# Kernel optimization log

Hardware: AMD Instinct MI355X
Metric: run time of the kernel (lower is better)

## Reference

```python
import jax, jax.numpy as jnp
import numpy as np

K_TOTAL = 48
NUM_RINGS = 3
RING_K = K_TOTAL // NUM_RINGS
RADIUS = 50.0
NUM_HEADS = 4


def setup_inputs() -> dict:
    key = jax.random.key(0)
    ks = jax.random.split(key, 12)
    B, N, Fin, D = 2, 4096, 256, 256
    H = D // 2
    features = jax.random.normal(ks[0], (B, N, Fin), jnp.float32)
    xy = jax.random.uniform(ks[1], (B, N, 2), jnp.float32) * 200.0
    t = jax.random.uniform(ks[2], (B, N, 1), jnp.float32) * 100.0
    coords = jnp.concatenate([xy, t], -1)

    def lin(k, fan_out, fan_in):
        bound = 1.0 / np.sqrt(fan_in)
        kw, kb = jax.random.split(k)
        W = jax.random.uniform(kw, (fan_out, fan_in), jnp.float32, -bound, bound)
        b = jax.random.uniform(kb, (fan_out,), jnp.float32, -bound, bound)
        return W, b

    Wfeat, bfeat = lin(ks[3], D, Fin)
    Wpe1, bpe1 = lin(ks[4], H, 4)
    Wpe2, bpe2 = lin(ks[5], D, H)
    Win, bin_ = lin(ks[6], 3 * D, D)
    Wout, bout = lin(ks[7], D, D)
    Wg1, bg1 = lin(ks[8], 32, 4)
    Wg2, bg2 = lin(ks[9], NUM_RINGS, 32)
    gamma = jnp.ones((D,), jnp.float32)
    beta = jnp.zeros((D,), jnp.float32)
    return dict(features=features, coords=coords, Wfeat=Wfeat, bfeat=bfeat,
                Wpe1=Wpe1, bpe1=bpe1, Wpe2=Wpe2, bpe2=bpe2,
                Win=Win, bin_=bin_, Wout=Wout, bout=bout,
                Wg1=Wg1, bg1=bg1, Wg2=Wg2, bg2=bg2, gamma=gamma, beta=beta)


def _safe_norm(x):
    # median over a size-1 last dim equals x itself (matches torch path)
    denom = jnp.median(x, axis=-1, keepdims=True) + 1e-6
    return jnp.clip(x / denom, 0.0, 10.0)


def _encode_one(bf, bc, p):
    N, D = bf.shape
    inf = jnp.float32(jnp.inf)
    # --- pairwise KNN: spatial + 0.3*|dt|, causal + radius + no-self ---
    diff = bc[:, None, :] - bc[None, :, :]                  # (N,N,3)
    sd = jnp.sqrt(jnp.sum(diff[..., :2] ** 2, -1))          # (N,N)
    dist = sd + 0.3 * jnp.abs(diff[..., 2])
    t = bc[:, 2]
    bad = jnp.eye(N, dtype=bool) | (t[None, :] > t[:, None]) | (sd > RADIUS)
    dist = jnp.where(bad, inf, dist)
    neg_top, idx = jax.lax.top_k(-dist, K_TOTAL)            # K smallest
    kdist_raw = -neg_top                                    # (N,K) ascending
    valid = jnp.isfinite(kdist_raw)
    kdist = jnp.where(valid, kdist_raw, 0.0)
    # --- neighbor gather + relative positional encoding ---
    neigh = bf[idx]                                         # (N,K,D)
    ncoord = bc[idx]                                        # (N,K,3)
    rel = jnp.concatenate([ncoord - bc[:, None, :], kdist[..., None]], -1)
    pe = jax.nn.relu(rel @ p['Wpe1'].T + p['bpe1']) @ p['Wpe2'].T + p['bpe2']
    neigh = neigh + pe
    # --- per-ring masked MHA (shared weights across rings) ---
    R, Kr, Hh = NUM_RINGS, RING_K, NUM_HEADS
    hd = D // Hh
    kr = neigh.reshape(N, R, Kr, D)
    vr = valid.reshape(N, R, Kr)
    Wq, Wk, Wv = p['Win'][:D], p['Win'][D:2 * D], p['Win'][2 * D:]
    bq, bk, bv = p['bin_'][:D], p['bin_'][D:2 * D], p['bin_'][2 * D:]
    q = (bf @ Wq.T + bq).reshape(N, Hh, hd) / jnp.sqrt(jnp.float32(hd))
    k = (kr @ Wk.T + bk).reshape(N, R, Kr, Hh, hd)
    v = (kr @ Wv.T + bv).reshape(N, R, Kr, Hh, hd)
    logits = jnp.einsum('nhd,nrkhd->nrhk', q, k)
    logits = jnp.where(vr[:, :, None, :], logits, -1e9)
    attn = jax.nn.softmax(logits, axis=-1)
    out = jnp.einsum('nrhk,nrkhd->nrhd', attn, v).reshape(N, R, D)
    out = out @ p['Wout'].T + p['bout']
    ring_any = vr.any(-1)                                   # (N,R)
    aggs = jnp.where(ring_any[..., None], out, 0.0)
    # --- ring gate from local density / time structure ---
    vc = jnp.maximum(valid.sum(-1), 1)                      # (N,)
    dens = jnp.take_along_axis(kdist, (vc - 1)[:, None], axis=1)
    dens_n = _safe_norm(dens)[:, 0]
    ratio = jnp.clip(vc.astype(jnp.float32) / K_TOTAL, 0.0, 1.0)
    dt = jnp.abs(ncoord[..., 2] - t[:, None])
    dtm = jnp.where(valid, dt, 0.0)
    denom = vc.astype(jnp.float32)
    dt_mean = dtm.sum(-1) / denom
    dt_sq = jnp.where(valid, (dt - dt_mean[:, None]) ** 2, 0.0)
    dt_std = jnp.sqrt(dt_sq.sum(-1) / denom + 1e-8)
    gate_in = jnp.stack([dens_n, ratio,
                         _safe_norm(dt_mean[:, None])[:, 0],
                         _safe_norm(dt_std[:, None])[:, 0]], -1)
    glog = jax.nn.relu(gate_in @ p['Wg1'].T + p['bg1']) @ p['Wg2'].T + p['bg2']
    glog = jnp.where(ring_any, glog, -inf)
    no_nb = ~ring_any.any(-1)
    special = jnp.where(jnp.arange(R) == 0, 10.0, 0.0).astype(jnp.float32)
    glog = jnp.where(no_nb[:, None], special[None, :], glog)
    w = jax.nn.softmax(glog, axis=-1)
    fused = jnp.einsum('nr,nrd->nd', w, aggs)
    # --- residual + layernorm (dropout is identity in eval) ---
    x = bf + fused
    mu = x.mean(-1, keepdims=True)
    var = x.var(-1, keepdims=True)
    return (x - mu) / jnp.sqrt(var + 1e-5) * p['gamma'] + p['beta']


def reference(features, coords, Wfeat, bfeat, Wpe1, bpe1, Wpe2, bpe2,
              Win, bin_, Wout, bout, Wg1, bg1, Wg2, bg2, gamma, beta):
    p = dict(Wpe1=Wpe1, bpe1=bpe1, Wpe2=Wpe2, bpe2=bpe2, Win=Win, bin_=bin_,
             Wout=Wout, bout=bout, Wg1=Wg1, bg1=bg1, Wg2=Wg2, bg2=bg2,
             gamma=gamma, beta=beta)
    feat_proj = features @ Wfeat.T + bfeat                  # (B,N,D)
    return jax.vmap(lambda f, c: _encode_one(f, c, p))(feat_proj, coords)
```

## Files before the change

### kernel.cpp

```cpp
#include <hip/hip_runtime.h>
#include <cmath>

#define NPTS 4096
#define NB   8192
#define DM   256
#define KK   48

__global__ __launch_bounds__(128) void prep_wkv2(
    const float* __restrict__ Win, const float* __restrict__ Wpe2,
    const float* __restrict__ bpe2, const float* __restrict__ bin_,
    float* __restrict__ Wk2, float* __restrict__ Wv2,
    float* __restrict__ bkf, float* __restrict__ bvf)
{
    const int o = blockIdx.x;
    const int j = threadIdx.x;
    const float* wk = Win + (size_t)(256 + o) * 256;
    const float* wv = Win + (size_t)(512 + o) * 256;
    float ak = 0.f, av = 0.f;
    for (int d = 0; d < 256; ++d) {
        float pw = Wpe2[(size_t)d * 128 + j];
        ak = fmaf(wk[d], pw, ak);
        av = fmaf(wv[d], pw, av);
    }
    Wk2[(size_t)o * 128 + j] = ak;
    Wv2[(size_t)o * 128 + j] = av;

    __shared__ float pk[128], pv[128];
    pk[j] = wk[j] * bpe2[j] + wk[j + 128] * bpe2[j + 128];
    pv[j] = wv[j] * bpe2[j] + wv[j + 128] * bpe2[j + 128];
    __syncthreads();
    for (int off = 64; off >= 1; off >>= 1) {
        if (j < off) { pk[j] += pk[j + off]; pv[j] += pv[j + off]; }
        __syncthreads();
    }
    if (j == 0) {
        bkf[o] = bin_[256 + o] + pk[0];
        bvf[o] = bin_[512 + o] + pv[0];
    }
}

__global__ __launch_bounds__(256) void prep_wqw2(
    const float* __restrict__ Win, const float* __restrict__ Wk2,
    const float* __restrict__ bin_,
    float* __restrict__ WqW2, float* __restrict__ bqW2)
{
    const int o = blockIdx.x;
    const int h = o >> 7, j = o & 127;
    const int d = threadIdx.x;
    float acc = 0.f;
    for (int dp = 0; dp < 64; ++dp) {
        const float w2 = Wk2[(size_t)(64 * h + dp) * 128 + j];
        acc = fmaf(Win[(size_t)(64 * h + dp) * 256 + d], w2, acc);
    }
    WqW2[(size_t)o * 256 + d] = acc * 0.125f;
    if (d < 64) {
        float pb = bin_[64 * h + d] * Wk2[(size_t)(64 * h + d) * 128 + j];
        #pragma unroll
        for (int off = 1; off < 64; off <<= 1) pb += __shfl_xor(pb, off);
        if (d == 0) bqW2[o] = pb * 0.125f;
    }
}

__global__ __launch_bounds__(256) void prep_wcat(
    const float* __restrict__ Wout, const float* __restrict__ Wv2,
    float* __restrict__ Wcat)
{
    const int o = blockIdx.x;
    const int t = threadIdx.x;
    Wcat[(size_t)o * 768 + t] = Wout[(size_t)o * 256 + t];
    for (int v = t; v < 512; v += 256) {
        const int h = v >> 7, jj = v & 127;
        const float* wo  = Wout + (size_t)o * 256 + h * 64;
        const float* wv2 = Wv2 + (size_t)(h * 64) * 128 + jj;
        float a = 0.f;
        for (int dp = 0; dp < 64; ++dp) a = fmaf(wo[dp], wv2[(size_t)dp * 128], a);
        Wcat[(size_t)o * 768 + 256 + v] = a;
    }
}

#define GEMM_BODY(XPTR, XSTRIDE, WPTR, KDIM, R0, C0)                          \
    __shared__ float xs[32][65];                                              \
    __shared__ float wsd[32][65];                                             \
    const int tid = threadIdx.x;                                              \
    const int lm = tid >> 5, lk = tid & 31;                                   \
    const int rr = 4 * (tid & 15), cc = 4 * (tid >> 4);                       \
    float acc[4][4] = {{0.f,0.f,0.f,0.f},{0.f,0.f,0.f,0.f},                   \
                       {0.f,0.f,0.f,0.f},{0.f,0.f,0.f,0.f}};                  \
    for (int k0 = 0; k0 < (KDIM); k0 += 32) {                                 \
        __syncthreads();                                                      \
        _Pragma("unroll")                                                     \
        for (int it = 0; it < 8; ++it) {                                      \
            const int m = lm + it * 8;                                        \
            xs[lk][m]  = (XPTR)[(size_t)((R0) + m) * (XSTRIDE) + k0 + lk];    \
            wsd[lk][m] = (WPTR)[(size_t)((C0) + m) * (KDIM) + k0 + lk];       \
        }                                                                     \
        __syncthreads();                                                      \
        _Pragma("unroll")                                                     \
        for (int k = 0; k < 32; ++k) {                                        \
            const float4 xv = *(const float4*)&xs[k][rr];                     \
            const float4 wv = *(const float4*)&wsd[k][cc];                    \
            acc[0][0] = fmaf(xv.x, wv.x, acc[0][0]);                          \
            acc[0][1] = fmaf(xv.x, wv.y, acc[0][1]);                          \
            acc[0][2] = fmaf(xv.x, wv.z, acc[0][2]);                          \
            acc[0][3] = fmaf(xv.x, wv.w, acc[0][3]);                          \
            acc[1][0] = fmaf(xv.y, wv.x, acc[1][0]);                          \
            acc[1][1] = fmaf(xv.y, wv.y, acc[1][1]);                          \
            acc[1][2] = fmaf(xv.y, wv.z, acc[1][2]);                          \
            acc[1][3] = fmaf(xv.y, wv.w, acc[1][3]);                          \
            acc[2][0] = fmaf(xv.z, wv.x, acc[2][0]);                          \
            acc[2][1] = fmaf(xv.z, wv.y, acc[2][1]);                          \
            acc[2][2] = fmaf(xv.z, wv.z, acc[2][2]);                          \
            acc[2][3] = fmaf(xv.z, wv.w, acc[2][3]);                          \
            acc[3][0] = fmaf(xv.w, wv.x, acc[3][0]);                          \
            acc[3][1] = fmaf(xv.w, wv.y, acc[3][1]);                          \
            acc[3][2] = fmaf(xv.w, wv.z, acc[3][2]);                          \
            acc[3][3] = fmaf(xv.w, wv.w, acc[3][3]);                          \
        }                                                                     \
    }

__global__ __launch_bounds__(256) void gemm_plain(
    const float* __restrict__ X, int xstride,
    const float* __restrict__ W, const float* __restrict__ bias,
    float scale, float* __restrict__ Y, int ystride, int K, int ntiles)
{
    const int bid = blockIdx.x;
    const int r0 = (bid / ntiles) * 64;
    const int c0 = (bid % ntiles) * 64;
    GEMM_BODY(X, xstride, W, K, r0, c0)
    float b0 = 0.f, b1 = 0.f, b2 = 0.f, b3 = 0.f;
    if (bias) { b0 = bias[c0+cc+0]; b1 = bias[c0+cc+1]; b2 = bias[c0+cc+2]; b3 = bias[c0+cc+3]; }
    #pragma unroll
    for (int i = 0; i < 4; ++i) {
        float4 o;
        o.x = (acc[i][0] + b0) * scale;
        o.y = (acc[i][1] + b1) * scale;
        o.z = (acc[i][2] + b2) * scale;
        o.w = (acc[i][3] + b3) * scale;
        *(float4*)&Y[(size_t)(r0 + rr + i) * ystride + c0 + cc] = o;
    }
}

__global__ __launch_bounds__(256) void gemm_qkvw(
    const float* __restrict__ feat, const float* __restrict__ Win,
    const float* __restrict__ WqW2,
    const float* __restrict__ bin_, const float* __restrict__ bkf,
    const float* __restrict__ bvf, const float* __restrict__ bqW2,
    float* __restrict__ Qm, float* __restrict__ Kp,
    float* __restrict__ Vp, float* __restrict__ qWa)
{
    const int bid = blockIdx.x;
    const int r0 = (bid / 20) * 64;
    const int cg = (bid % 20) * 64;
    const float* Wb; const float* bb; float scale; float* Yb; int ys; int c0;
    if (cg < 256)      { Wb = Win;             bb = bin_; scale = 0.125f; Yb = Qm;  ys = 256; c0 = cg; }
    else if (cg < 512) { Wb = Win + 256 * 256; bb = bkf;  scale = 1.f;    Yb = Kp;  ys = 256; c0 = cg - 256; }
    else if (cg < 768) { Wb = Win + 512 * 256; bb = bvf;  scale = 1.f;    Yb = Vp;  ys = 256; c0 = cg - 512; }
    else               { Wb = WqW2;            bb = bqW2; scale = 1.f;    Yb = qWa; ys = 512; c0 = cg - 768; }
    GEMM_BODY(feat, 256, Wb, 256, r0, c0)
    const float b0 = bb[c0+cc+0], b1 = bb[c0+cc+1], b2 = bb[c0+cc+2], b3 = bb[c0+cc+3];
    #pragma unroll
    for (int i = 0; i < 4; ++i) {
        float4 o;
        o.x = (acc[i][0] + b0) * scale;
        o.y = (acc[i][1] + b1) * scale;
        o.z = (acc[i][2] + b2) * scale;
        o.w = (acc[i][3] + b3) * scale;
        *(float4*)&Yb[(size_t)(r0 + rr + i) * ys + c0 + cc] = o;
    }
}

#define GRPMIN(BASE, OUTKEY) do {                                            \
    unsigned m_ = 0xFFFFFFFFu; int ms_ = (BASE);                             \
    _Pragma("unroll")                                                        \
    for (int s_ = 0; s_ < 16; ++s_) {                                        \
        unsigned v_ = ((dead >> ((BASE) + s_)) & 1ull) ? 0xFFFFFFFFu         \
                                                       : db[(BASE) + s_];    \
        if (v_ < m_) { m_ = v_; ms_ = (BASE) + s_; }                         \
    }                                                                        \
    OUTKEY = ((unsigned long long)m_ << 32) | (unsigned)(ms_ * 64 + lane);   \
} while (0)

static __device__ __forceinline__ unsigned long long umin64(
    unsigned long long a, unsigned long long b) { return a < b ? a : b; }

static __device__ __forceinline__ unsigned long long shfl_xor_u64(
    unsigned long long v, int mask)
{
    unsigned lo = (unsigned)(v & 0xFFFFFFFFull);
    unsigned hi = (unsigned)(v >> 32);
    lo = (unsigned)__shfl_xor((int)lo, mask);
    hi = (unsigned)__shfl_xor((int)hi, mask);
    return ((unsigned long long)hi << 32) | lo;
}

__global__ __launch_bounds__(256) void knn_kernel(
    const float* __restrict__ coords, int* __restrict__ nidx, float* __restrict__ ndist)
{
    #pragma clang fp contract(off)
    const int lane = threadIdx.x & 63;
    const int p = blockIdx.x * 4 + (threadIdx.x >> 6);
    const int b = p >> 12;
    const int i = p & 4095;
    const float* cb = coords + (size_t)b * NPTS * 3;
    const float xi = cb[i * 3 + 0], yi = cb[i * 3 + 1], ti = cb[i * 3 + 2];

    unsigned db[64];
    #pragma unroll
    for (int s = 0; s < 64; ++s) {
        const int j = s * 64 + lane;
        const float xj = cb[j * 3 + 0], yj = cb[j * 3 + 1], tj = cb[j * 3 + 2];
        const float dx = xi - xj, dy = yi - yj;
        const float sd = sqrtf(dx * dx + dy * dy);
        const float dd = sd + 0.3f * fabsf(tj - ti);
        const bool bad = (j == i) || (tj > ti) || (sd > 50.0f);
        db[s] = bad ? 0x7F800000u : __float_as_uint(dd);
    }

    unsigned long long dead = 0ull;
    unsigned long long k0, k1, k2, k3;
    GRPMIN(0,  k0); GRPMIN(16, k1); GRPMIN(32, k2); GRPMIN(48, k3);
    unsigned long long lmin = umin64(umin64(k0, k1), umin64(k2, k3));

    unsigned long long reskey = 0ull;
    for (int k = 0; k < KK; ++k) {
        unsigned long long kb = lmin;
        #pragma unroll
        for (int off = 1; off < 64; off <<= 1) {
            unsigned long long o = shfl_xor_u64(kb, off);
            kb = o < kb ? o : kb;
        }
        if (lane == k) reskey = kb;
        const int wj = (int)(kb & 0xFFFFFFFFull);
        if ((wj & 63) == lane) {
            const int ws = wj >> 6;
            dead |= (1ull << ws);
            const int g = ws >> 4;
            if      (g == 0) GRPMIN(0,  k0);
            else if (g == 1) GRPMIN(16, k1);
            else if (g == 2) GRPMIN(32, k2);
            else             GRPMIN(48, k3);
            lmin = umin64(umin64(k0, k1), umin64(k2, k3));
        }
    }

    if (lane < KK) {
        ndist[(size_t)p * KK + lane] = __uint_as_float((unsigned)(reskey >> 32));
        nidx [(size_t)p * KK + lane] = (int)(reskey & 0xFFFFFFFFull);
    }
}

__global__ __launch_bounds__(256) void attn_kernel(
    const float* __restrict__ coords, const float* __restrict__ Q,
    const float* __restrict__ Kp, const float* __restrict__ Vp,
    const float* __restrict__ qWa,
    const int* __restrict__ nidx, const float* __restrict__ ndist,
    const float* __restrict__ Wpe1, const float* __restrict__ bpe1,
    const float* __restrict__ Wg1, const float* __restrict__ bg1,
    const float* __restrict__ Wg2, const float* __restrict__ bg2,
    float* __restrict__ vh, unsigned char* __restrict__ nonb)
{
    const int p = blockIdx.x;
    const int b = p >> 12;
    const int i = p & 4095;
    const int tid = threadIdx.x;

    __shared__ __align__(16) float qs[4][68];
    __shared__ __align__(16) float qw[4][132];
    __shared__ __align__(16) float rel[KK][4];
    __shared__ float kd[KK];
    __shared__ int   sidx[KK];
    __shared__ int   svalid[KK];
    __shared__ __align__(16) float hid[KK][132];
    __shared__ float wsh[KK][4];
    __shared__ float wring[4];

    for (int v = tid; v < 256; v += 256) qs[v >> 6][v & 63] = Q[(size_t)p * 256 + v];
    for (int v = tid; v < 512; v += 256) qw[v >> 7][v & 127] = qWa[(size_t)p * 512 + v];
    const float* cb = coords + (size_t)b * NPTS * 3;
    const float xi = cb[i * 3 + 0], yi = cb[i * 3 + 1], ti = cb[i * 3 + 2];
    if (tid < KK) {
        const float dd = ndist[(size_t)p * KK + tid];
        const int ix = nidx[(size_t)p * KK + tid];
        sidx[tid] = ix;
        const int val = (dd < 3.0e38f) ? 1 : 0;
        svalid[tid] = val;
        const float kdd = val ? dd : 0.f;
        kd[tid] = kdd;
        rel[tid][0] = cb[ix * 3 + 0] - xi;
        rel[tid][1] = cb[ix * 3 + 1] - yi;
        rel[tid][2] = cb[ix * 3 + 2] - ti;
        rel[tid][3] = kdd;
    }
    __syncthreads();

    if (tid < 64) {
        const int val = (tid < KK) ? svalid[tid] : 0;
        float dtv = 0.f;
        if (tid < KK && val) dtv = fabsf(rel[tid][2]);
        const unsigned long long m = __ballot(val != 0);
        const int count = __popcll(m);
        const int vc = count > 0 ? count : 1;
        float sdt = dtv;
        #pragma unroll
        for (int off = 1; off < 64; off <<= 1) sdt += __shfl_xor(sdt, off);
        const float vcf = (float)vc;
        const float dtmean = sdt / vcf;
        float dq = 0.f;
        if (tid < KK && val) { float tq = dtv - dtmean; dq = tq * tq; }
        float sdq = dq;
        #pragma unroll
        for (int off = 1; off < 64; off <<= 1) sdq += __shfl_xor(sdq, off);
        const float dtstd = sqrtf(sdq / vcf + 1e-8f);
        const float dens = kd[vc - 1];
        const float g0 = fminf(fmaxf(dens / (dens + 1e-6f), 0.f), 10.f);
        const float g1v = fminf(fmaxf(vcf / 48.f, 0.f), 1.f);
        const float g2 = fminf(fmaxf(dtmean / (dtmean + 1e-6f), 0.f), 10.f);
        const float g3 = fminf(fmaxf(dtstd / (dtstd + 1e-6f), 0.f), 10.f);
        float gh = 0.f;
        if (tid < 32) {
            gh = bg1[tid] + g0 * Wg1[tid * 4 + 0] + g1v * Wg1[tid * 4 + 1]
               + g2 * Wg1[tid * 4 + 2] + g3 * Wg1[tid * 4 + 3];
            gh = fmaxf(gh, 0.f);
        }
        float gl[3];
        #pragma unroll
        for (int r = 0; r < 3; ++r) {
            float part = (tid < 32) ? gh * Wg2[r * 32 + tid] : 0.f;
            #pragma unroll
            for (int off = 1; off < 64; off <<= 1) part += __shfl_xor(part, off);
            gl[r] = part + bg2[r];
        }
        if (count < 1)  gl[0] = -INFINITY;
        if (count < 17) gl[1] = -INFINITY;
        if (count < 33) gl[2] = -INFINITY;
        float w0 = 0.f, w1 = 0.f, w2 = 0.f;
        if (count > 0) {
            const float mx = fmaxf(gl[0], fmaxf(gl[1], gl[2]));
            const float e0 = expf(gl[0] - mx), e1 = expf(gl[1] - mx), e2 = expf(gl[2] - mx);
            const float es = e0 + e1 + e2;
            w0 = e0 / es; w1 = e1 / es; w2 = e2 / es;
        }
        if (tid == 0) {
            wring[0] = w0; wring[1] = w1; wring[2] = w2;
            nonb[p] = (count == 0) ? (unsigned char)1 : (unsigned char)0;
        }
    }
    for (int v = tid; v < KK * 128; v += 256) {
        const int s = v >> 7, jj = v & 127;
        const float4 r4 = *(const float4*)(&rel[s][0]);
        const float4 w4 = *(const float4*)(Wpe1 + (size_t)jj * 4);
        float hdd = bpe1[jj] + r4.x * w4.x + r4.y * w4.y + r4.z * w4.z + r4.w * w4.w;
        hid[s][jj] = fmaxf(hdd, 0.f);
    }
    __syncthreads();

    if (tid < 192) {
        const int s_ = tid >> 2, h_ = tid & 3;
        float acc = 0.f;
        const float4* hp = (const float4*)(&hid[s_][0]);
        const float4* qp = (const float4*)(&qw[h_][0]);
        #pragma unroll
        for (int j4 = 0; j4 < 32; ++j4) {
            float4 hv = hp[j4], qv = qp[j4];
            acc = fmaf(qv.x, hv.x, fmaf(qv.y, hv.y, fmaf(qv.z, hv.z, fmaf(qv.w, hv.w, acc))));
        }
        const float* kr = Kp + ((size_t)b * NPTS + sidx[s_]) * 256 + h_ * 64;
        const float4* qsp = (const float4*)(&qs[h_][0]);
        #pragma unroll
        for (int d4 = 0; d4 < 16; ++d4) {
            float4 kv = *(const float4*)(kr + d4 * 4);
            float4 qv = qsp[d4];
            acc = fmaf(qv.x, kv.x, fmaf(qv.y, kv.y, fmaf(qv.z, kv.z, fmaf(qv.w, kv.w, acc))));
        }
        float logit = svalid[s_] ? acc : -1e9f;
        float mx = logit;
        #pragma unroll
        for (int off = 4; off < 64; off <<= 1) mx = fmaxf(mx, __shfl_xor(mx, off));
        const float e = expf(logit - mx);
        float es = e;
        #pragma unroll
        for (int off = 4; off < 64; off <<= 1) es += __shfl_xor(es, off);
        wsh[s_][h_] = (e / es) * wring[tid >> 6];
    }
    __syncthreads();

    {
        const int h = tid >> 6, dp = tid & 63;
        const size_t bb = (size_t)b * NPTS;
        const float* vpb = Vp + h * 64 + dp;
        float a0 = 0.f, a1 = 0.f, a2 = 0.f, a3 = 0.f;
        #pragma unroll
        for (int s = 0; s < 12; ++s) {
            a0 = fmaf(wsh[s     ][h], vpb[(bb + sidx[s     ]) * 256], a0);
            a1 = fmaf(wsh[s + 12][h], vpb[(bb + sidx[s + 12]) * 256], a1);
            a2 = fmaf(wsh[s + 24][h], vpb[(bb + sidx[s + 24]) * 256], a2);
            a3 = fmaf(wsh[s + 36][h], vpb[(bb + sidx[s + 36]) * 256], a3);
        }
        vh[(size_t)p * 768 + tid] = (a0 + a1) + (a2 + a3);
    }
    for (int v = tid; v < 512; v += 256) {
        const int h = v >> 7, jj = v & 127;
        float a0 = 0.f, a1 = 0.f;
        #pragma unroll
        for (int s = 0; s < 24; ++s) {
            a0 = fmaf(wsh[s     ][h], hid[s     ][jj], a0);
            a1 = fmaf(wsh[s + 24][h], hid[s + 24][jj], a1);
        }
        vh[(size_t)p * 768 + 256 + v] = a0 + a1;
    }
}

__global__ __launch_bounds__(256) void ln_kernel(
    const float* __restrict__ xo, const float* __restrict__ feat,
    const float* __restrict__ bout, const unsigned char* __restrict__ nonb,
    const float* __restrict__ gamma, const float* __restrict__ beta,
    float* __restrict__ out)
{
    const int lane = threadIdx.x & 63;
    const int p = blockIdx.x * 4 + (threadIdx.x >> 6);
    const float4 xv = *(const float4*)&xo  [(size_t)p * 256 + lane * 4];
    const float4 fv = *(const float4*)&feat[(size_t)p * 256 + lane * 4];
    const float4 bv = *(const float4*)&bout[lane * 4];
    const float bm = nonb[p] ? 0.f : 1.f;
    float x0 = xv.x + fv.x + bm * bv.x;
    float x1 = xv.y + fv.y + bm * bv.y;
    float x2 = xv.z + fv.z + bm * bv.z;
    float x3 = xv.w + fv.w + bm * bv.w;
    float s1 = x0 + x1 + x2 + x3;
    float s2 = fmaf(x0, x0, fmaf(x1, x1, fmaf(x2, x2, x3 * x3)));
    #pragma unroll
    for (int off = 1; off < 64; off <<= 1) {
        s1 += __shfl_xor(s1, off);
        s2 += __shfl_xor(s2, off);
    }
    const float mu = s1 * (1.f / 256.f);
    const float var = s2 * (1.f / 256.f) - mu * mu;
    const float rs = 1.f / sqrtf(var + 1e-5f);
    const float4 gv = *(const float4*)&gamma[lane * 4];
    const float4 tv = *(const float4*)&beta [lane * 4];
    float4 o;
    o.x = (x0 - mu) * rs * gv.x + tv.x;
    o.y = (x1 - mu) * rs * gv.y + tv.y;
    o.z = (x2 - mu) * rs * gv.z + tv.z;
    o.w = (x3 - mu) * rs * gv.w + tv.w;
    *(float4*)&out[(size_t)p * 256 + lane * 4] = o;
}

extern "C" void kernel_launch(void* const* d_in, const int* in_sizes, int n_in,
                              void* d_out, int out_size, void* d_ws, size_t ws_size,
                              hipStream_t stream) {
    (void)in_sizes; (void)n_in; (void)out_size; (void)ws_size;
    const float* features = (const float*)d_in[0];
    const float* coords   = (const float*)d_in[1];
    const float* Wfeat    = (const float*)d_in[2];
    const float* bfeat    = (const float*)d_in[3];
    const float* Wpe1     = (const float*)d_in[4];
    const float* bpe1     = (const float*)d_in[5];
    const float* Wpe2     = (const float*)d_in[6];
    const float* bpe2     = (const float*)d_in[7];
    const float* Win      = (const float*)d_in[8];
    const float* bin_     = (const float*)d_in[9];
    const float* Wout     = (const float*)d_in[10];
    const float* bout     = (const float*)d_in[11];
    const float* Wg1      = (const float*)d_in[12];
    const float* bg1      = (const float*)d_in[13];
    const float* Wg2      = (const float*)d_in[14];
    const float* bg2      = (const float*)d_in[15];
    const float* gamma    = (const float*)d_in[16];
    const float* beta     = (const float*)d_in[17];
    float* out = (float*)d_out;

    float* ws   = (float*)d_ws;
    float* feat = ws;
    float* Qm   = feat + (size_t)NB * DM;
    float* Kp   = Qm   + (size_t)NB * DM;
    float* Vp   = Kp   + (size_t)NB * DM;
    float* qWa  = Vp   + (size_t)NB * DM;
    float* vh   = qWa  + (size_t)NB * 512;
    float* Wk2  = vh   + (size_t)NB * 768;
    float* Wv2  = Wk2  + 256 * 128;
    float* Wcat = Wv2  + 256 * 128;
    float* WqW2 = Wcat + 256 * 768;
    float* bkf  = WqW2 + 512 * 256;
    float* bvf  = bkf + 256;
    float* bqW2 = bvf + 256;
    float* ndist = bqW2 + 512;
    int*   nidx = (int*)(ndist + (size_t)NB * KK);
    unsigned char* nonb = (unsigned char*)(nidx + (size_t)NB * KK);
    float* xo   = Qm;

    prep_wkv2<<<256, 128, 0, stream>>>(Win, Wpe2, bpe2, bin_, Wk2, Wv2, bkf, bvf);
    prep_wqw2<<<512, 256, 0, stream>>>(Win, Wk2, bin_, WqW2, bqW2);
    prep_wcat<<<256, 256, 0, stream>>>(Wout, Wv2, Wcat);

    gemm_plain<<<(NB / 64) * 4, 256, 0, stream>>>(
        features, 256, Wfeat, bfeat, 1.0f, feat, 256, 256, 4);

    gemm_qkvw<<<(NB / 64) * 20, 256, 0, stream>>>(
        feat, Win, WqW2, bin_, bkf, bvf, bqW2, Qm, Kp, Vp, qWa);

    knn_kernel<<<NB / 4, 256, 0, stream>>>(coords, nidx, ndist);

    attn_kernel<<<NB, 256, 0, stream>>>(coords, Qm, Kp, Vp, qWa, nidx, ndist,
                                        Wpe1, bpe1, Wg1, bg1, Wg2, bg2, vh, nonb);

    gemm_plain<<<(NB / 64) * 4, 256, 0, stream>>>(
        vh, 768, Wcat, nullptr, 1.0f, xo, 256, 768, 4);

    ln_kernel<<<NB / 4, 256, 0, stream>>>(xo, feat, bout, nonb, gamma, beta, out);
}
```

Before: 606.4 us.

## Replace wave-wide shuffle reduction in KNN with per-16-lane DPP top-k and merge

Each 16-lane row now finds its own 48 smallest keys using four DPP min steps, replacing the six cross-lane shuffle steps that spanned the whole wavefront. The four sorted per-row lists go to shared memory and are merged by rank, with each candidate's position found by binary search across the four lists before writing. This aims to cut the latency of each of the 48 selection iterations. In exchange it adds shared memory, a block barrier and a merge phase, and correctness depends on the DPP control codes covering a full 16-lane row.

```diff
diff --git a/kernel.cpp b/kernel.cpp
--- a/kernel.cpp
+++ b/kernel.cpp
@@ -169,6 +169,7 @@
     }
 }
 
+
 #define GRPMIN(BASE, OUTKEY) do {                                            \
     unsigned m_ = 0xFFFFFFFFu; int ms_ = (BASE);                             \
     _Pragma("unroll")                                                        \
@@ -183,22 +184,27 @@
 static __device__ __forceinline__ unsigned long long umin64(
     unsigned long long a, unsigned long long b) { return a < b ? a : b; }
 
-static __device__ __forceinline__ unsigned long long shfl_xor_u64(
-    unsigned long long v, int mask)
-{
-    unsigned lo = (unsigned)(v & 0xFFFFFFFFull);
-    unsigned hi = (unsigned)(v >> 32);
-    lo = (unsigned)__shfl_xor((int)lo, mask);
-    hi = (unsigned)__shfl_xor((int)hi, mask);
-    return ((unsigned long long)hi << 32) | lo;
-}
+#define DPP_MIN_STEP(K, CTRL) do {                                           \
+    unsigned lo_ = (unsigned)((K) & 0xFFFFFFFFull);                          \
+    unsigned hi_ = (unsigned)((K) >> 32);                                    \
+    unsigned plo_ = (unsigned)__builtin_amdgcn_update_dpp(                   \
+        (int)lo_, (int)lo_, (CTRL), 0xF, 0xF, false);                        \
+    unsigned phi_ = (unsigned)__builtin_amdgcn_update_dpp(                   \
+        (int)hi_, (int)hi_, (CTRL), 0xF, 0xF, false);                        \
+    unsigned long long o_ = ((unsigned long long)phi_ << 32) | plo_;         \
+    (K) = o_ < (K) ? o_ : (K);                                               \
+} while (0)
 
 __global__ __launch_bounds__(256) void knn_kernel(
     const float* __restrict__ coords, int* __restrict__ nidx, float* __restrict__ ndist)
 {
     #pragma clang fp contract(off)
-    const int lane = threadIdx.x & 63;
-    const int p = blockIdx.x * 4 + (threadIdx.x >> 6);
+    const int tid = threadIdx.x;
+    const int lane = tid & 63;
+    const int wv = tid >> 6;
+    const int ll = lane & 15;
+    const int g  = lane >> 4;
+    const int p = blockIdx.x * 4 + wv;
     const int b = p >> 12;
     const int i = p & 4095;
     const float* cb = coords + (size_t)b * NPTS * 3;
@@ -221,31 +227,48 @@
     GRPMIN(0,  k0); GRPMIN(16, k1); GRPMIN(32, k2); GRPMIN(48, k3);
     unsigned long long lmin = umin64(umin64(k0, k1), umin64(k2, k3));
 
-    unsigned long long reskey = 0ull;
+    __shared__ unsigned long long gk[4][4][64];
+    gk[wv][g][48 + ll] = 0xFFFFFFFFFFFFFFFFull;
+
     for (int k = 0; k < KK; ++k) {
         unsigned long long kb = lmin;
-        #pragma unroll
-        for (int off = 1; off < 64; off <<= 1) {
-            unsigned long long o = shfl_xor_u64(kb, off);
-            kb = o < kb ? o : kb;
-        }
-        if (lane == k) reskey = kb;
+        DPP_MIN_STEP(kb, 0x0B1);
+        DPP_MIN_STEP(kb, 0x04E);
+        DPP_MIN_STEP(kb, 0x141);
+        DPP_MIN_STEP(kb, 0x140);
+        if (ll == (k & 15)) gk[wv][g][k] = kb;
         const int wj = (int)(kb & 0xFFFFFFFFull);
         if ((wj & 63) == lane) {
             const int ws = wj >> 6;
             dead |= (1ull << ws);
-            const int g = ws >> 4;
-            if      (g == 0) GRPMIN(0,  k0);
-            else if (g == 1) GRPMIN(16, k1);
-            else if (g == 2) GRPMIN(32, k2);
-            else             GRPMIN(48, k3);
+            const int gg = ws >> 4;
+            if      (gg == 0) GRPMIN(0,  k0);
+            else if (gg == 1) GRPMIN(16, k1);
+            else if (gg == 2) GRPMIN(32, k2);
+            else              GRPMIN(48, k3);
             lmin = umin64(umin64(k0, k1), umin64(k2, k3));
         }
     }
-
-    if (lane < KK) {
-        ndist[(size_t)p * KK + lane] = __uint_as_float((unsigned)(reskey >> 32));
-        nidx [(size_t)p * KK + lane] = (int)(reskey & 0xFFFFFFFFull);
+    __syncthreads();
+
+    #pragma unroll
+    for (int e = 0; e < 3; ++e) {
+        const int myi = ll + e * 16;
+        const unsigned long long key = gk[wv][g][myi];
+        int rank = 0;
+        #pragma unroll
+        for (int gg = 0; gg < 4; ++gg) {
+            const unsigned long long* arr = &gk[wv][gg][0];
+            int c = 0;
+            #pragma unroll
+            for (int s = 32; s >= 1; s >>= 1)
+                if (arr[c + s - 1] < key) c += s;
+            rank += c;
+        }
+        if (rank < KK) {
+            ndist[(size_t)p * KK + rank] = __uint_as_float((unsigned)(key >> 32));
+            nidx [(size_t)p * KK + rank] = (int)(key & 0xFFFFFFFFull);
+        }
     }
 }
 
```

Result: slower. 694.4 us (+14.5%).
